# Optimization experiments

Hardware: AMD Instinct MI355X
Metric: run time of the kernel (lower is better)

The kernel has to match this reference:

```python
import jax, jax.numpy as jnp
import numpy as np

N_EMBEDS = 1024
N_HEADS = 16
EPS = 1e-3


def layer_norm(x, gamma, beta):
    mean = jnp.mean(x, axis=-1, keepdims=True)
    var = jnp.mean((x - mean) ** 2, axis=-1, keepdims=True)
    return gamma * (x - mean) / jnp.sqrt(var + EPS) + beta


def setup_inputs() -> dict:
    key = jax.random.key(0)
    ks = jax.random.split(key, 8)
    B, T, C = 4, 2048, N_EMBEDS
    s = 1.0 / np.sqrt(C)
    return {
        "x": jax.random.normal(ks[0], (B, T, C), dtype=jnp.float32),
        "w_qkv": jax.random.normal(ks[1], (C, 3 * C), dtype=jnp.float32) * s,
        "w_proj": jax.random.normal(ks[2], (C, C), dtype=jnp.float32) * s,
        "b_proj": jnp.zeros((C,), dtype=jnp.float32),
        "w1": jax.random.normal(ks[3], (C, 4 * C), dtype=jnp.float32) * s,
        "b1": jnp.zeros((4 * C,), dtype=jnp.float32),
        "w2": jax.random.normal(ks[4], (4 * C, C), dtype=jnp.float32) * (0.5 / np.sqrt(C)),
        "b2": jnp.zeros((C,), dtype=jnp.float32),
        "gamma1": jnp.ones((C,), dtype=jnp.float32),
        "beta1": jnp.zeros((C,), dtype=jnp.float32),
        "gamma2": jnp.ones((C,), dtype=jnp.float32),
        "beta2": jnp.zeros((C,), dtype=jnp.float32),
    }


def reference(x, w_qkv, w_proj, b_proj, w1, b1, w2, b2, gamma1, beta1, gamma2, beta2):
    B, T, C = x.shape
    H = N_HEADS
    D = C // H
    scale = D ** -0.5

    # --- attention sub-layer (pre-LN) ---
    h = layer_norm(x, gamma1, beta1)
    qkv = h @ w_qkv                      # [B,T,3C]
    q, k, v = jnp.split(qkv, 3, axis=-1)
    q = q.reshape(B, T, H, D).transpose(0, 2, 1, 3)  # [B,H,T,D]
    k = k.reshape(B, T, H, D).transpose(0, 2, 1, 3)
    v = v.reshape(B, T, H, D).transpose(0, 2, 1, 3)
    att = jnp.einsum('bhqd,bhkd->bhqk', q, k) * scale
    causal = jnp.tril(jnp.ones((T, T), dtype=bool))
    att = jnp.where(causal[None, None], att, jnp.float32(-1e9))
    att = jax.nn.softmax(att, axis=-1)
    out = jnp.einsum('bhqk,bhkd->bhqd', att, v)
    out = out.transpose(0, 2, 1, 3).reshape(B, T, C)
    x = x + out @ w_proj + b_proj

    # --- FFN sub-layer (pre-LN, erf-GELU) ---
    h = layer_norm(x, gamma2, beta2)
    h = jax.nn.gelu(h @ w1 + b1, approximate=False)
    x = x + h @ w2 + b2
    return x
```

## Files before the change

### kernel.cpp

```cpp
#include <hip/hip_runtime.h>
#include <hip/hip_bf16.h>
#include <cstdint>
#include <cstddef>

#define B_ 4
#define T_ 2048
#define C_ 1024
#define H_ 16
#define D_ 64
#define M_ (B_*T_)

using bf16_t = __hip_bfloat16;
typedef __bf16 v8bf __attribute__((ext_vector_type(8)));
typedef float  v4f  __attribute__((ext_vector_type(4)));
typedef float  f32x16 __attribute__((ext_vector_type(16)));

#define QSCALE (0.125f * 1.44269504088896340736f)

static __device__ __forceinline__ bf16_t f2bf(float v){ return __float2bfloat16(v); }
static __device__ __forceinline__ float bfraw2f(unsigned short u){
  union { unsigned int i; float f; } c; c.i = ((unsigned int)u) << 16; return c.f;
}

static __device__ __forceinline__ void glds16(const bf16_t* g, bf16_t* l){
  __builtin_amdgcn_global_load_lds((__attribute__((address_space(1))) void*)g,
                                   (__attribute__((address_space(3))) void*)l, 16, 0, 0);
}

static __device__ __forceinline__ uint32_t cvt_pk_bf16(float lo, float hi){
  uint32_t w;
  asm("v_cvt_pk_bf16_f32 %0, %1, %2" : "=v"(w) : "v"(lo), "v"(hi));
  return w;
}

__global__ void k_transpose_cast(const float* __restrict__ in, bf16_t* __restrict__ out,
                                 int K, int N){
  __shared__ float tile[32][33];
  int k0 = blockIdx.y*32, n0 = blockIdx.x*32;
  int tx = threadIdx.x, ty = threadIdx.y;
  #pragma unroll
  for(int j=0;j<32;j+=8) tile[ty+j][tx] = in[(size_t)(k0+ty+j)*N + n0+tx];
  __syncthreads();
  #pragma unroll
  for(int j=0;j<32;j+=8) out[(size_t)(n0+ty+j)*K + k0+tx] = f2bf(tile[tx][ty+j]);
}

__global__ __launch_bounds__(256) void k_layernorm(const float* __restrict__ x,
                                                   const float* __restrict__ gamma,
                                                   const float* __restrict__ beta,
                                                   bf16_t* __restrict__ out){
  int row = blockIdx.x;
  int tid = threadIdx.x;
  const float4 v = reinterpret_cast<const float4*>(x + (size_t)row*C_)[tid];
  float s  = v.x+v.y+v.z+v.w;
  float ss = v.x*v.x+v.y*v.y+v.z*v.z+v.w*v.w;
  #pragma unroll
  for(int m=1;m<64;m<<=1){ s += __shfl_xor(s,m); ss += __shfl_xor(ss,m); }
  __shared__ float sbuf[4], ssbuf[4];
  int wid = tid>>6, lane = tid&63;
  if(lane==0){ sbuf[wid]=s; ssbuf[wid]=ss; }
  __syncthreads();
  s  = sbuf[0]+sbuf[1]+sbuf[2]+sbuf[3];
  ss = ssbuf[0]+ssbuf[1]+ssbuf[2]+ssbuf[3];
  float mean = s * (1.0f/C_);
  float var  = ss * (1.0f/C_) - mean*mean;
  float rstd = rsqrtf(var + 1e-3f);
  const float4 g = reinterpret_cast<const float4*>(gamma)[tid];
  const float4 b = reinterpret_cast<const float4*>(beta)[tid];
  union { ushort4 u; bf16_t h[4]; } pk;
  pk.h[0] = f2bf(g.x*(v.x-mean)*rstd + b.x);
  pk.h[1] = f2bf(g.y*(v.y-mean)*rstd + b.y);
  pk.h[2] = f2bf(g.z*(v.z-mean)*rstd + b.z);
  pk.h[3] = f2bf(g.w*(v.w-mean)*rstd + b.w);
  *reinterpret_cast<ushort4*>(out + (size_t)row*C_ + tid*4) = pk.u;
}

__global__ __launch_bounds__(256)
void k_add2(const bf16_t* __restrict__ p0, const bf16_t* __restrict__ p1,
            const float* __restrict__ bias, float* out){
  const int row = blockIdx.x, tid = threadIdx.x;
  float4 xr = reinterpret_cast<const float4*>(out + (size_t)row*C_)[tid];
  const ushort4 a = reinterpret_cast<const ushort4*>(p0 + (size_t)row*C_)[tid];
  const ushort4 b = reinterpret_cast<const ushort4*>(p1 + (size_t)row*C_)[tid];
  const float4 g = reinterpret_cast<const float4*>(bias)[tid];
  xr.x += bfraw2f(a.x) + bfraw2f(b.x) + g.x;
  xr.y += bfraw2f(a.y) + bfraw2f(b.y) + g.y;
  xr.z += bfraw2f(a.z) + bfraw2f(b.z) + g.z;
  xr.w += bfraw2f(a.w) + bfraw2f(b.w) + g.w;
  reinterpret_cast<float4*>(out + (size_t)row*C_)[tid] = xr;
}

template<int MODE>
__global__ __launch_bounds__(512, 1)
void k_gemm9(const bf16_t* __restrict__ A, const bf16_t* __restrict__ Bt,
             const float* __restrict__ bias, const float* resid,
             void* out0, void* out1, void* out2,
             int N, int ld, int klen, int gx)
{
  __shared__ __align__(16) bf16_t As[2][2][128*64];
  __shared__ __align__(16) bf16_t Bs[2][2][128*64];
  const int tid = threadIdx.x, lane = tid & 63, w = tid >> 6;
  const int wm = w >> 2, wn = w & 3;

  const int nwg = gx * 32;
  const int orig = blockIdx.y * gx + blockIdx.x;
  const int swz = (orig & 7) * (nwg >> 3) + (orig >> 3);
  const int ct = swz % gx, rt = swz / gx;
  const int row0 = rt * 256, col0 = ct * 256;
  const int koff = blockIdx.z * klen;

  const int sswz = ((lane & 7) ^ ((lane >> 3) & 7)) * 8;
  const int srow = w * 8 + (lane >> 3);
  const bf16_t* Agb = A  + (size_t)(row0 + srow) * ld + koff + sswz;
  const bf16_t* Bgb = Bt + (size_t)(col0 + srow) * ld + koff + sswz;

  auto stageA = [&](int tt, int hh){
    const bf16_t* src = Agb + (size_t)(hh * 128) * ld + tt * 64;
    bf16_t* dst = &As[tt & 1][hh][w * 512];
    glds16(src, dst);
    glds16(src + (size_t)64 * ld, dst + 4096);
  };
  auto stageB = [&](int tt, int hh){
    const bf16_t* src = Bgb + (size_t)(hh * 128) * ld + tt * 64;
    bf16_t* dst = &Bs[tt & 1][hh][w * 512];
    glds16(src, dst);
    glds16(src + (size_t)64 * ld, dst + 4096);
  };

  v8bf af[4][2], bfv[4][2];
  v4f acc[8][4] = {};

  auto LDA = [&](int bb, int mh){
    const bf16_t* base = &As[bb][wm][0];
    #pragma unroll
    for (int m = 0; m < 4; ++m)
      #pragma unroll
      for (int kk = 0; kk < 2; ++kk) {
        const int r  = mh*64 + m*16 + (lane & 15);
        const int sl = (kk*4 + (lane >> 4)) ^ (lane & 7);
        af[m][kk] = *reinterpret_cast<const v8bf*>(base + r*64 + sl*8);
      }
  };
  auto LDB = [&](int bb){
    const bf16_t* base = &Bs[bb][wn >> 1][0];
    #pragma unroll
    for (int n = 0; n < 4; ++n)
      #pragma unroll
      for (int kk = 0; kk < 2; ++kk) {
        const int r  = (wn & 1)*64 + n*16 + (lane & 15);
        const int sl = (kk*4 + (lane >> 4)) ^ (lane & 7);
        bfv[n][kk] = *reinterpret_cast<const v8bf*>(base + r*64 + sl*8);
      }
  };

#define MFMA_Q(mh_, nh_) \
  __builtin_amdgcn_s_setprio(1); \
  _Pragma("unroll") \
  for (int kk = 0; kk < 2; ++kk) \
    _Pragma("unroll") \
    for (int m = 0; m < 4; ++m) \
      _Pragma("unroll") \
      for (int n = 0; n < 2; ++n) \
        acc[(mh_)*4+m][(nh_)*2+n] = __builtin_amdgcn_mfma_f32_16x16x32_bf16( \
            af[m][kk], bfv[(nh_)*2+n][kk], acc[(mh_)*4+m][(nh_)*2+n], 0,0,0); \
  __builtin_amdgcn_s_setprio(0);

#define BAR()   __builtin_amdgcn_s_barrier()
#define LGKM0() do { asm volatile("s_waitcnt lgkmcnt(0)" ::: "memory"); \
                     __builtin_amdgcn_sched_barrier(0); } while(0)

  stageA(0,0); stageA(0,1); stageB(0,0); stageB(0,1);
  stageB(1,0); stageB(1,1); stageA(1,0);
  asm volatile("s_waitcnt vmcnt(6)" ::: "memory");
  BAR();

  const int NP = (klen >> 6) >> 1;
  for (int j = 0; j < NP; ++j) {
    const int t2 = 2*j + 2, t3 = 2*j + 3;
    const bool more = (j + 1 < NP);
    LDA(0, 0); LDB(0);
    stageA(2*j + 1, 1);
    BAR(); LGKM0(); MFMA_Q(0, 0); BAR();
    if (more) stageB(t2, 0);
    BAR(); MFMA_Q(0, 1); BAR();
    LDA(0, 1);
    if (more) stageB(t2, 1);
    BAR(); LGKM0(); MFMA_Q(1, 0); BAR();
    if (more) { stageA(t2, 0); asm volatile("s_waitcnt vmcnt(6)" ::: "memory"); }
    else      {                asm volatile("s_waitcnt vmcnt(0)" ::: "memory"); }
    BAR(); MFMA_Q(1, 1); BAR();
    LDA(1, 0); LDB(1);
    if (more) stageA(t2, 1);
    BAR(); LGKM0(); MFMA_Q(0, 0); BAR();
    if (more) stageB(t3, 0);
    BAR(); MFMA_Q(0, 1); BAR();
    LDA(1, 1);
    if (more) stageB(t3, 1);
    BAR(); LGKM0(); MFMA_Q(1, 0); BAR();
    if (more) { stageA(t3, 0); asm volatile("s_waitcnt vmcnt(6)" ::: "memory"); }
    else      {                asm volatile("s_waitcnt vmcnt(0)" ::: "memory"); }
    BAR(); MFMA_Q(1, 1); BAR();
  }
#undef MFMA_Q
#undef BAR
#undef LGKM0

  #pragma unroll
  for (int mf = 0; mf < 8; ++mf) {
    const int rbase = row0 + wm*128 + mf*16 + (lane>>4)*4;
    #pragma unroll
    for (int nf = 0; nf < 4; ++nf) {
      const int c = col0 + wn*64 + nf*16 + (lane&15);
      #pragma unroll
      for (int i = 0; i < 4; ++i) {
        const int rr = rbase + i;
        float v = acc[mf][nf][i];
        if constexpr(MODE==0){
          const int sec = c >> 10, cc = c & 1023;
          const int h = cc >> 6, d = cc & 63;
          const int b = rr >> 11, t = rr & 2047;
          if(sec==0)      ((bf16_t*)out0)[((size_t)(b*H_ + h)*T_ + t)*D_ + d] = f2bf(v * QSCALE);
          else if(sec==1) ((bf16_t*)out1)[((size_t)(b*H_ + h)*T_ + t)*D_ + d] = f2bf(v);
          else            ((bf16_t*)out2)[((size_t)(b*H_ + h)*D_ + d)*T_ + t] = f2bf(v);
        } else if constexpr(MODE==2){
          float o = v + bias[c];
          o = 0.5f*o*(1.0f + erff(o*0.70710678118f));
          ((bf16_t*)out0)[(size_t)rr*N + c] = f2bf(o);
        } else {
          bf16_t* dst = blockIdx.z ? (bf16_t*)out1 : (bf16_t*)out0;
          dst[(size_t)rr*N + c] = f2bf(v);
        }
      }
    }
  }
}

__global__ __launch_bounds__(512, 1)
void k_gemm8(const bf16_t* __restrict__ A, const bf16_t* __restrict__ Bt,
             const float* __restrict__ bias, const float* resid,
             float* out0, int N, int K, int gx)
{
  __shared__ __align__(16) bf16_t As[2][256*64];
  __shared__ __align__(16) bf16_t Bs[3][128*64];
  const int tid = threadIdx.x, lane = tid & 63, w = tid >> 6;
  const int wm = w >> 1, wn = w & 1;

  const int nwg = gx * 32;
  const int orig = blockIdx.y * gx + blockIdx.x;
  const int swz = (orig & 7) * (nwg >> 3) + (orig >> 3);
  const int ct = swz % gx, rt = swz / gx;
  const int row0 = rt * 256, col0 = ct * 128;

  const int sswz = ((lane & 7) ^ ((lane >> 3) & 7)) * 8;
  const int srow = w * 8 + (lane >> 3);
  const bf16_t* Agb = A  + (size_t)(row0 + srow) * K + sswz;
  const bf16_t* Bgb = Bt + (size_t)(col0 + srow) * K + sswz;

  auto stageA = [&](int tt){
    const bf16_t* src = Agb + tt * 64;
    bf16_t* dst = &As[tt & 1][w * 512];
    #pragma unroll
    for (int i = 0; i < 4; ++i)
      glds16(src + (size_t)(i*64) * K, dst + i*4096);
  };
  auto stageB = [&](int tt){
    const bf16_t* src = Bgb + tt * 64;
    bf16_t* dst = &Bs[tt % 3][w * 512];
    #pragma unroll
    for (int i = 0; i < 2; ++i)
      glds16(src + (size_t)(i*64) * K, dst + i*4096);
  };

  v8bf af[4][2], bfv[4][2];
  v4f acc[4][4] = {};

  auto LDA = [&](int ab){
    const bf16_t* base = &As[ab][0];
    #pragma unroll
    for (int m = 0; m < 4; ++m)
      #pragma unroll
      for (int kk = 0; kk < 2; ++kk) {
        const int r  = wm*64 + m*16 + (lane & 15);
        const int sl = (kk*4 + (lane >> 4)) ^ (lane & 7);
        af[m][kk] = *reinterpret_cast<const v8bf*>(base + r*64 + sl*8);
      }
  };
  auto LDB = [&](int bb, int nh){
    const bf16_t* base = &Bs[bb][0];
    #pragma unroll
    for (int n = 0; n < 2; ++n)
      #pragma unroll
      for (int kk = 0; kk < 2; ++kk) {
        const int r  = wn*64 + (nh*2+n)*16 + (lane & 15);
        const int sl = (kk*4 + (lane >> 4)) ^ (lane & 7);
        bfv[nh*2+n][kk] = *reinterpret_cast<const v8bf*>(base + r*64 + sl*8);
      }
  };

#define MFMA_Q(nh_) \
  __builtin_amdgcn_s_setprio(1); \
  _Pragma("unroll") \
  for (int kk = 0; kk < 2; ++kk) \
    _Pragma("unroll") \
    for (int m = 0; m < 4; ++m) \
      _Pragma("unroll") \
      for (int n = 0; n < 2; ++n) \
        acc[m][(nh_)*2+n] = __builtin_amdgcn_mfma_f32_16x16x32_bf16( \
            af[m][kk], bfv[(nh_)*2+n][kk], acc[m][(nh_)*2+n], 0,0,0); \
  __builtin_amdgcn_s_setprio(0);

#define BAR()   __builtin_amdgcn_s_barrier()
#define LGKM0() do { asm volatile("s_waitcnt lgkmcnt(0)" ::: "memory"); \
                     __builtin_amdgcn_sched_barrier(0); } while(0)
#define VM6()   asm volatile("s_waitcnt vmcnt(6)" ::: "memory")
#define VM0()   asm volatile("s_waitcnt vmcnt(0)" ::: "memory")

  const int NP = (K >> 6) >> 1;
  stageB(0); stageA(0); stageB(1); stageA(1);
  VM6();
  BAR();

  for (int j = 0; j < NP; ++j) {
    const int t0 = 2*j, t1 = 2*j + 1, t2 = 2*j + 2, t3 = 2*j + 3;
    const bool more = (j + 1 < NP);
    LDA(0); LDB(t0 % 3, 0);
    if (more) stageB(t2);
    BAR(); LGKM0(); MFMA_Q(0); BAR();
    LDB(t0 % 3, 1);
    if (more) { stageA(t2); VM6(); } else { VM0(); }
    BAR(); LGKM0(); MFMA_Q(1); BAR();
    LDA(1); LDB(t1 % 3, 0);
    if (more) stageB(t3);
    BAR(); LGKM0(); MFMA_Q(0); BAR();
    LDB(t1 % 3, 1);
    if (more) { stageA(t3); VM6(); } else { VM0(); }
    BAR(); LGKM0(); MFMA_Q(1); BAR();
  }
#undef MFMA_Q
#undef BAR
#undef LGKM0
#undef VM6
#undef VM0

  #pragma unroll
  for (int mf = 0; mf < 4; ++mf) {
    const int rbase = row0 + wm*64 + mf*16 + (lane>>4)*4;
    #pragma unroll
    for (int nf = 0; nf < 4; ++nf) {
      const int c = col0 + wn*64 + nf*16 + (lane&15);
      #pragma unroll
      for (int i = 0; i < 4; ++i) {
        const int rr = rbase + i;
        out0[(size_t)rr*N + c] = acc[mf][nf][i] + bias[c] + resid[(size_t)rr*N + c];
      }
    }
  }
}

__global__ __launch_bounds__(256)
void k_attn(const bf16_t* __restrict__ Q, const bf16_t* __restrict__ Kg,
            const bf16_t* __restrict__ Vt, bf16_t* __restrict__ O)
{
  __shared__ __align__(16) bf16_t Ks [64][72];
  __shared__ __align__(16) bf16_t Vts[64][72];
  __shared__ __align__(16) bf16_t Os [128][72];
  const int bh = blockIdx.y;
  const int pair = blockIdx.x;
  const int tid = threadIdx.x, lane = tid & 63, w = tid >> 6;
  const int ql = lane & 31, hi = lane >> 5;
  const int srow = tid >> 2;
  const int scol = (tid & 3) * 16;
  const bf16_t* Kgp = Kg + ((size_t)bh*T_ + srow)*D_ + scol;
  const bf16_t* Vtp = Vt + ((size_t)bh*D_ + srow)*T_ + scol;
  const int b = bh >> 4, h = bh & 15;

  for(int half=0; half<2; ++half){
    const int qt = half ? pair : (15 - pair);
    const int qbase = qt*128 + w*32;
    const int q = qbase + ql;

    v8bf qf[4];
    {
      const bf16_t* Qb = Q + ((size_t)bh*T_ + q)*D_ + hi*8;
      #pragma unroll
      for(int ds=0; ds<4; ds++)
        qf[ds] = *reinterpret_cast<const v8bf*>(Qb + ds*16);
    }

    f32x16 accO[2] = {};
    float mrun = -1e30f, lrun = 0.0f;
    const int NT = (qt + 1) * 2;

    v8bf kr0 = *reinterpret_cast<const v8bf*>(Kgp);
    v8bf kr1 = *reinterpret_cast<const v8bf*>(Kgp + 8);
    v8bf vr0 = *reinterpret_cast<const v8bf*>(Vtp);
    v8bf vr1 = *reinterpret_cast<const v8bf*>(Vtp + 8);

    for(int t=0; t<NT; t++){
      const int kv0 = t*64;
      *reinterpret_cast<v8bf*>(&Ks [srow][scol  ]) = kr0;
      *reinterpret_cast<v8bf*>(&Ks [srow][scol+8]) = kr1;
      *reinterpret_cast<v8bf*>(&Vts[srow][scol  ]) = vr0;
      *reinterpret_cast<v8bf*>(&Vts[srow][scol+8]) = vr1;
      __syncthreads();
      if(t+1 < NT){
        const size_t kn = (size_t)(kv0 + 64);
        kr0 = *reinterpret_cast<const v8bf*>(Kgp + kn*D_);
        kr1 = *reinterpret_cast<const v8bf*>(Kgp + kn*D_ + 8);
        vr0 = *reinterpret_cast<const v8bf*>(Vtp + kn);
        vr1 = *reinterpret_cast<const v8bf*>(Vtp + kn + 8);
      }

      if(kv0 <= qbase + 31){
        f32x16 sT[2] = {};
        #pragma unroll
        for(int kvh=0; kvh<2; kvh++)
          #pragma unroll
          for(int ds=0; ds<4; ds++){
            v8bf kf = *reinterpret_cast<const v8bf*>(&Ks[kvh*32 + ql][ds*16 + hi*8]);
            sT[kvh] = __builtin_amdgcn_mfma_f32_32x32x16_bf16(kf, qf[ds], sT[kvh], 0,0,0);
          }

        if(kv0 + 63 > qbase){
          const int qrel = q - kv0 - hi*4;
          #pragma unroll
          for(int kvh=0; kvh<2; kvh++)
            #pragma unroll
            for(int r=0; r<16; r++){
              const int c = kvh*32 + (r&3) + 8*(r>>2);
              if(c > qrel) sT[kvh][r] = -1e30f;
            }
        }

        float pm = sT[0][0];
        #pragma unroll
        for(int r=1; r<16; r++) pm = fmaxf(pm, sT[0][r]);
        #pragma unroll
        for(int r=0; r<16; r++) pm = fmaxf(pm, sT[1][r]);
        pm = fmaxf(pm, __shfl_xor(pm, 32));

        if(__any(pm - mrun > 8.0f)){
          const float mnew = fmaxf(mrun, pm);
          const float corr = __builtin_amdgcn_exp2f(mrun - mnew);
          mrun = mnew;
          lrun *= corr;
          #pragma unroll
          for(int dh=0; dh<2; dh++)
            #pragma unroll
            for(int r=0; r<16; r++) accO[dh][r] *= corr;
        }

        float rs = 0.0f;
        #pragma unroll
        for(int kvh=0; kvh<2; kvh++)
          #pragma unroll
          for(int r=0; r<16; r++){
            float p = __builtin_amdgcn_exp2f(sT[kvh][r] - mrun);
            sT[kvh][r] = p;
            rs += p;
          }
        rs += __shfl_xor(rs, 32);
        lrun += rs;

        v8bf pfrag[4];
        #pragma unroll
        for(int s4=0; s4<4; s4++){
          const int kvh = s4>>1, bb = (s4&1)*8;
          uint32_t wa = cvt_pk_bf16(sT[kvh][bb+0], sT[kvh][bb+1]);
          uint32_t wb = cvt_pk_bf16(sT[kvh][bb+2], sT[kvh][bb+3]);
          uint32_t wc = cvt_pk_bf16(sT[kvh][bb+4], sT[kvh][bb+5]);
          uint32_t wd = cvt_pk_bf16(sT[kvh][bb+6], sT[kvh][bb+7]);
          uint32_t xwa = (uint32_t)__shfl_xor((int)wa, 32);
          uint32_t xwb = (uint32_t)__shfl_xor((int)wb, 32);
          uint32_t xwc = (uint32_t)__shfl_xor((int)wc, 32);
          uint32_t xwd = (uint32_t)__shfl_xor((int)wd, 32);
          union { uint32_t u[4]; v8bf v; } pk;
          pk.u[0] = hi ? xwc : wa;
          pk.u[1] = hi ? xwd : wb;
          pk.u[2] = hi ? wc  : xwa;
          pk.u[3] = hi ? wd  : xwb;
          pfrag[s4] = pk.v;
        }

        #pragma unroll
        for(int dh=0; dh<2; dh++)
          #pragma unroll
          for(int s4=0; s4<4; s4++){
            v8bf vf = *reinterpret_cast<const v8bf*>(&Vts[dh*32 + ql][s4*16 + hi*8]);
            accO[dh] = __builtin_amdgcn_mfma_f32_32x32x16_bf16(vf, pfrag[s4], accO[dh], 0,0,0);
          }
      }
      __syncthreads();
    }

    const float inv = 1.0f / lrun;
    #pragma unroll
    for(int dh=0; dh<2; dh++)
      #pragma unroll
      for(int rg=0; rg<4; rg++){
        uint32_t lo_ = cvt_pk_bf16(accO[dh][rg*4+0]*inv, accO[dh][rg*4+1]*inv);
        uint32_t hi_ = cvt_pk_bf16(accO[dh][rg*4+2]*inv, accO[dh][rg*4+3]*inv);
        uint2 w2; w2.x = lo_; w2.y = hi_;
        *reinterpret_cast<uint2*>(&Os[w*32 + ql][dh*32 + rg*8 + hi*4]) = w2;
      }
    __syncthreads();
    const int orow = tid >> 1, ocol = (tid & 1) * 32;
    bf16_t* Og = O + ((size_t)(b*T_ + qt*128 + orow))*C_ + h*64 + ocol;
    #pragma unroll
    for(int j=0;j<4;j++)
      *reinterpret_cast<v8bf*>(Og + j*8) = *reinterpret_cast<const v8bf*>(&Os[orow][ocol + j*8]);
    __syncthreads();
  }
}

extern "C" void kernel_launch(void* const* d_in, const int* in_sizes, int n_in,
                              void* d_out, int out_size, void* d_ws, size_t ws_size,
                              hipStream_t stream) {
  const float* x      = (const float*)d_in[0];
  const float* w_qkv  = (const float*)d_in[1];
  const float* w_proj = (const float*)d_in[2];
  const float* b_proj = (const float*)d_in[3];
  const float* w1     = (const float*)d_in[4];
  const float* b1     = (const float*)d_in[5];
  const float* w2     = (const float*)d_in[6];
  const float* b2     = (const float*)d_in[7];
  const float* gamma1 = (const float*)d_in[8];
  const float* beta1  = (const float*)d_in[9];
  const float* gamma2 = (const float*)d_in[10];
  const float* beta2  = (const float*)d_in[11];

  char* ws = (char*)d_ws;
  bf16_t* wqkv_t  = (bf16_t*)(ws + 0);
  bf16_t* wproj_t = (bf16_t*)(ws + 6291456);
  bf16_t* w1_t    = (bf16_t*)(ws + 8388608);
  bf16_t* w2_t    = (bf16_t*)(ws + 16777216);
  bf16_t* qb      = (bf16_t*)(ws + 25165824);
  bf16_t* kb      = (bf16_t*)(ws + 41943040);
  bf16_t* vtb     = (bf16_t*)(ws + 58720256);
  bf16_t* obuf    = (bf16_t*)(ws + 75497472);
  bf16_t* hb      = (bf16_t*)(ws + 92274688);
  bf16_t* gb      = (bf16_t*)(ws + 25165824);
  float*  x2      = (float*)d_out;

  dim3 tb(32,8);
  k_transpose_cast<<<dim3(3072/32, 1024/32), tb, 0, stream>>>(w_qkv,  wqkv_t, 1024, 3072);
  k_transpose_cast<<<dim3(1024/32, 1024/32), tb, 0, stream>>>(w_proj, wproj_t,1024, 1024);
  k_transpose_cast<<<dim3(4096/32, 1024/32), tb, 0, stream>>>(w1,     w1_t,   1024, 4096);
  k_transpose_cast<<<dim3(1024/32, 4096/32), tb, 0, stream>>>(w2,     w2_t,   4096, 1024);

  k_layernorm<<<M_, 256, 0, stream>>>(x, gamma1, beta1, hb);

  k_gemm9<0><<<dim3(12, 32, 1), 512, 0, stream>>>(hb, wqkv_t, nullptr, nullptr,
                                                  qb, kb, vtb, 3072, 1024, 1024, 12);
  k_attn<<<dim3(8, B_*H_), 256, 0, stream>>>(qb, kb, vtb, obuf);

  k_gemm8<<<dim3(8, 32), 512, 0, stream>>>(obuf, wproj_t, b_proj, x,
                                           x2, 1024, 1024, 8);
  k_layernorm<<<M_, 256, 0, stream>>>(x2, gamma2, beta2, hb);

  k_gemm9<2><<<dim3(16, 32, 1), 512, 0, stream>>>(hb, w1_t, b1, nullptr,
                                                  gb, nullptr, nullptr, 4096, 1024, 1024, 16);
  k_gemm9<4><<<dim3(4, 32, 2), 512, 0, stream>>>(gb, w2_t, nullptr, nullptr,
                                                 obuf, hb, nullptr, 1024, 4096, 2048, 4);
  k_add2<<<M_, 256, 0, stream>>>(obuf, hb, b2, x2);
}
```

Baseline: 404.8 us.

## Make gemm9 persistent and prefetch the next tile during the epilogue

Turns the bf16 GEMM kernel into a persistent kernel. It launches 256 blocks (one per CU) that loop over output tiles with a grid stride. While each block runs the epilogue stores for the current tile, it already issues the prologue global-to-LDS loads for the next tile, which hides the epilogue behind memory traffic and avoids a partial final wave. A risk is the LDS buffer reuse: the prologue overwrites buffers 0 and 1 while the last MFMAs may still be reading LDS, and the tile-to-block mapping changes L2 locality.

Result: no change. 402.8 us (-0.5%).

```diff
diff --git a/kernel.cpp b/kernel.cpp
--- a/kernel.cpp
+++ b/kernel.cpp
@@ -95,24 +95,26 @@
 void k_gemm9(const bf16_t* __restrict__ A, const bf16_t* __restrict__ Bt,
              const float* __restrict__ bias, const float* resid,
              void* out0, void* out1, void* out2,
-             int N, int ld, int klen, int gx)
+             int N, int ld, int klen, int gx, int tc)
 {
   __shared__ __align__(16) bf16_t As[2][2][128*64];
   __shared__ __align__(16) bf16_t Bs[2][2][128*64];
   const int tid = threadIdx.x, lane = tid & 63, w = tid >> 6;
   const int wm = w >> 2, wn = w & 3;
-
-  const int nwg = gx * 32;
-  const int orig = blockIdx.y * gx + blockIdx.x;
-  const int swz = (orig & 7) * (nwg >> 3) + (orig >> 3);
-  const int ct = swz % gx, rt = swz / gx;
-  const int row0 = rt * 256, col0 = ct * 256;
   const int koff = blockIdx.z * klen;
 
   const int sswz = ((lane & 7) ^ ((lane >> 3) & 7)) * 8;
   const int srow = w * 8 + (lane >> 3);
-  const bf16_t* Agb = A  + (size_t)(row0 + srow) * ld + koff + sswz;
-  const bf16_t* Bgb = Bt + (size_t)(col0 + srow) * ld + koff + sswz;
+
+  int row0, col0;
+  const bf16_t *Agb, *Bgb;
+  auto set_tile = [&](int tile){
+    const int swz = (tile & 7) * (tc >> 3) + (tile >> 3);
+    const int ct = swz % gx, rt = swz / gx;
+    row0 = rt * 256; col0 = ct * 256;
+    Agb = A  + (size_t)(row0 + srow) * ld + koff + sswz;
+    Bgb = Bt + (size_t)(col0 + srow) * ld + koff + sswz;
+  };
 
   auto stageA = [&](int tt, int hh){
     const bf16_t* src = Agb + (size_t)(hh * 128) * ld + tt * 64;
@@ -126,9 +128,13 @@
     glds16(src, dst);
     glds16(src + (size_t)64 * ld, dst + 4096);
   };
+  auto stage_prologue = [&](){
+    stageA(0,0); stageA(0,1); stageB(0,0); stageB(0,1);
+    stageB(1,0); stageB(1,1); stageA(1,0);
+  };
 
   v8bf af[4][2], bfv[4][2];
-  v4f acc[8][4] = {};
+  v4f acc[8][4];
 
   auto LDA = [&](int bb, int mh){
     const bf16_t* base = &As[bb][wm][0];
@@ -169,70 +175,86 @@
 #define LGKM0() do { asm volatile("s_waitcnt lgkmcnt(0)" ::: "memory"); \
                      __builtin_amdgcn_sched_barrier(0); } while(0)
 
-  stageA(0,0); stageA(0,1); stageB(0,0); stageB(0,1);
-  stageB(1,0); stageB(1,1); stageA(1,0);
-  asm volatile("s_waitcnt vmcnt(6)" ::: "memory");
-  BAR();
-
   const int NP = (klen >> 6) >> 1;
-  for (int j = 0; j < NP; ++j) {
-    const int t2 = 2*j + 2, t3 = 2*j + 3;
-    const bool more = (j + 1 < NP);
-    LDA(0, 0); LDB(0);
-    stageA(2*j + 1, 1);
-    BAR(); LGKM0(); MFMA_Q(0, 0); BAR();
-    if (more) stageB(t2, 0);
-    BAR(); MFMA_Q(0, 1); BAR();
-    LDA(0, 1);
-    if (more) stageB(t2, 1);
-    BAR(); LGKM0(); MFMA_Q(1, 0); BAR();
-    if (more) { stageA(t2, 0); asm volatile("s_waitcnt vmcnt(6)" ::: "memory"); }
-    else      {                asm volatile("s_waitcnt vmcnt(0)" ::: "memory"); }
-    BAR(); MFMA_Q(1, 1); BAR();
-    LDA(1, 0); LDB(1);
-    if (more) stageA(t2, 1);
-    BAR(); LGKM0(); MFMA_Q(0, 0); BAR();
-    if (more) stageB(t3, 0);
-    BAR(); MFMA_Q(0, 1); BAR();
-    LDA(1, 1);
-    if (more) stageB(t3, 1);
-    BAR(); LGKM0(); MFMA_Q(1, 0); BAR();
-    if (more) { stageA(t3, 0); asm volatile("s_waitcnt vmcnt(6)" ::: "memory"); }
-    else      {                asm volatile("s_waitcnt vmcnt(0)" ::: "memory"); }
-    BAR(); MFMA_Q(1, 1); BAR();
+  int tile = blockIdx.x;
+  set_tile(tile);
+  stage_prologue();
+
+  for (;;) {
+    asm volatile("s_waitcnt vmcnt(0)" ::: "memory");
+    BAR();
+    #pragma unroll
+    for (int mf = 0; mf < 8; ++mf)
+      #pragma unroll
+      for (int nf = 0; nf < 4; ++nf)
+        acc[mf][nf] = (v4f){0.f, 0.f, 0.f, 0.f};
+
+    for (int j = 0; j < NP; ++j) {
+      const int t2 = 2*j + 2, t3 = 2*j + 3;
+      const bool more = (j + 1 < NP);
+      LDA(0, 0); LDB(0);
+      stageA(2*j + 1, 1);
+      BAR(); LGKM0(); MFMA_Q(0, 0); BAR();
+      if (more) stageB(t2, 0);
+      BAR(); MFMA_Q(0, 1); BAR();
+      LDA(0, 1);
+      if (more) stageB(t2, 1);
+      BAR(); LGKM0(); MFMA_Q(1, 0); BAR();
+      if (more) { stageA(t2, 0); asm volatile("s_waitcnt vmcnt(6)" ::: "memory"); }
+      else      {                asm volatile("s_waitcnt vmcnt(0)" ::: "memory"); }
+      BAR(); MFMA_Q(1, 1); BAR();
+      LDA(1, 0); LDB(1);
+      if (more) stageA(t2, 1);
+      BAR(); LGKM0(); MFMA_Q(0, 0); BAR();
+      if (more) stageB(t3, 0);
+      BAR(); MFMA_Q(0, 1); BAR();
+      LDA(1, 1);
+      if (more) stageB(t3, 1);
+      BAR(); LGKM0(); MFMA_Q(1, 0); BAR();
+      if (more) { stageA(t3, 0); asm volatile("s_waitcnt vmcnt(6)" ::: "memory"); }
+      else      {                asm volatile("s_waitcnt vmcnt(0)" ::: "memory"); }
+      BAR(); MFMA_Q(1, 1); BAR();
+    }
+
+    const int erow0 = row0, ecol0 = col0;
+    const int next = tile + (int)gridDim.x;
+    const bool have_next = (next < tc);
+    if (have_next) { set_tile(next); stage_prologue(); }
+
+    #pragma unroll
+    for (int mf = 0; mf < 8; ++mf) {
+      const int rbase = erow0 + wm*128 + mf*16 + (lane>>4)*4;
+      #pragma unroll
+      for (int nf = 0; nf < 4; ++nf) {
+        const int c = ecol0 + wn*64 + nf*16 + (lane&15);
+        #pragma unroll
+        for (int i = 0; i < 4; ++i) {
+          const int rr = rbase + i;
+          float v = acc[mf][nf][i];
+          if constexpr(MODE==0){
+            const int sec = c >> 10, cc = c & 1023;
+            const int h = cc >> 6, d = cc & 63;
+            const int b = rr >> 11, t = rr & 2047;
+            if(sec==0)      ((bf16_t*)out0)[((size_t)(b*H_ + h)*T_ + t)*D_ + d] = f2bf(v * QSCALE);
+            else if(sec==1) ((bf16_t*)out1)[((size_t)(b*H_ + h)*T_ + t)*D_ + d] = f2bf(v);
+            else            ((bf16_t*)out2)[((size_t)(b*H_ + h)*D_ + d)*T_ + t] = f2bf(v);
+          } else if constexpr(MODE==2){
+            float o = v + bias[c];
+            o = 0.5f*o*(1.0f + erff(o*0.70710678118f));
+            ((bf16_t*)out0)[(size_t)rr*N + c] = f2bf(o);
+          } else {
+            bf16_t* dst = blockIdx.z ? (bf16_t*)out1 : (bf16_t*)out0;
+            dst[(size_t)rr*N + c] = f2bf(v);
+          }
+        }
+      }
+    }
+    if (!have_next) break;
+    tile = next;
   }
 #undef MFMA_Q
 #undef BAR
 #undef LGKM0
-
-  #pragma unroll
-  for (int mf = 0; mf < 8; ++mf) {
-    const int rbase = row0 + wm*128 + mf*16 + (lane>>4)*4;
-    #pragma unroll
-    for (int nf = 0; nf < 4; ++nf) {
-      const int c = col0 + wn*64 + nf*16 + (lane&15);
-      #pragma unroll
-      for (int i = 0; i < 4; ++i) {
-        const int rr = rbase + i;
-        float v = acc[mf][nf][i];
-        if constexpr(MODE==0){
-          const int sec = c >> 10, cc = c & 1023;
-          const int h = cc >> 6, d = cc & 63;
-          const int b = rr >> 11, t = rr & 2047;
-          if(sec==0)      ((bf16_t*)out0)[((size_t)(b*H_ + h)*T_ + t)*D_ + d] = f2bf(v * QSCALE);
-          else if(sec==1) ((bf16_t*)out1)[((size_t)(b*H_ + h)*T_ + t)*D_ + d] = f2bf(v);
-          else            ((bf16_t*)out2)[((size_t)(b*H_ + h)*D_ + d)*T_ + t] = f2bf(v);
-        } else if constexpr(MODE==2){
-          float o = v + bias[c];
-          o = 0.5f*o*(1.0f + erff(o*0.70710678118f));
-          ((bf16_t*)out0)[(size_t)rr*N + c] = f2bf(o);
-        } else {
-          bf16_t* dst = blockIdx.z ? (bf16_t*)out1 : (bf16_t*)out0;
-          dst[(size_t)rr*N + c] = f2bf(v);
-        }
-      }
-    }
-  }
 }
 
 __global__ __launch_bounds__(512, 1)
@@ -550,17 +572,17 @@
 
   k_layernorm<<<M_, 256, 0, stream>>>(x, gamma1, beta1, hb);
 
-  k_gemm9<0><<<dim3(12, 32, 1), 512, 0, stream>>>(hb, wqkv_t, nullptr, nullptr,
-                                                  qb, kb, vtb, 3072, 1024, 1024, 12);
+  k_gemm9<0><<<dim3(256, 1, 1), 512, 0, stream>>>(hb, wqkv_t, nullptr, nullptr,
+                                                  qb, kb, vtb, 3072, 1024, 1024, 12, 384);
   k_attn<<<dim3(8, B_*H_), 256, 0, stream>>>(qb, kb, vtb, obuf);
 
   k_gemm8<<<dim3(8, 32), 512, 0, stream>>>(obuf, wproj_t, b_proj, x,
                                            x2, 1024, 1024, 8);
   k_layernorm<<<M_, 256, 0, stream>>>(x2, gamma2, beta2, hb);
 
-  k_gemm9<2><<<dim3(16, 32, 1), 512, 0, stream>>>(hb, w1_t, b1, nullptr,
-                                                  gb, nullptr, nullptr, 4096, 1024, 1024, 16);
-  k_gemm9<4><<<dim3(4, 32, 2), 512, 0, stream>>>(gb, w2_t, nullptr, nullptr,
-                                                 obuf, hb, nullptr, 1024, 4096, 2048, 4);
+  k_gemm9<2><<<dim3(256, 1, 1), 512, 0, stream>>>(hb, w1_t, b1, nullptr,
+                                                  gb, nullptr, nullptr, 4096, 1024, 1024, 16, 512);
+  k_gemm9<4><<<dim3(128, 1, 2), 512, 0, stream>>>(gb, w2_t, nullptr, nullptr,
+                                                  obuf, hb, nullptr, 1024, 4096, 2048, 4, 128);
   k_add2<<<M_, 256, 0, stream>>>(obuf, hb, b2, x2);
 }
```
